# Kernel tuning notes

Hardware: AMD Instinct MI355X
Metric: run time of the kernel (lower is better)

The kernel has to match this reference:

```python
import jax, jax.numpy as jnp
import numpy as np

N_NODES = 200000
N_EDGES = 6400000
D_IN, D_HID, D_OUT = 128, 16, 172


def gcn_conv(x, edge_index, W, b, n):
    """PyG GCNConv: add self-loops, symmetric D^-1/2 A D^-1/2 normalization,
    linear projection, scatter-add aggregation, bias."""
    src, dst = edge_index[0], edge_index[1]
    loops = jnp.arange(n, dtype=edge_index.dtype)
    src = jnp.concatenate([src, loops])
    dst = jnp.concatenate([dst, loops])
    # in-degree with self-loops (>= 1, so rsqrt is safe)
    deg = jax.ops.segment_sum(jnp.ones_like(dst, dtype=x.dtype), dst, num_segments=n)
    dinv = jax.lax.rsqrt(deg)
    lin = x @ W  # [n, d_out]
    norm = dinv[src] * dinv[dst]  # per-edge normalization
    msg = lin[src] * norm[:, None]  # gather + scale
    out = jax.ops.segment_sum(msg, dst, num_segments=n)  # scatter-add
    return out + b


def setup_inputs() -> dict:
    key = jax.random.key(0)
    k1, k2, k3, k4, k5, k6 = jax.random.split(key, 6)
    x = jax.random.normal(k1, (N_NODES, D_IN), dtype=jnp.float32)
    edge_index = jax.random.randint(k2, (2, N_EDGES), 0, N_NODES, dtype=jnp.int64)
    W1 = jax.random.normal(k3, (D_IN, D_HID), dtype=jnp.float32) * (1.0 / np.sqrt(D_IN))
    b1 = jnp.zeros((D_HID,), dtype=jnp.float32)
    W2 = jax.random.normal(k4, (D_HID, D_OUT), dtype=jnp.float32) * (1.0 / np.sqrt(D_HID))
    b2 = jnp.zeros((D_OUT,), dtype=jnp.float32)
    return {"x": x, "edge_index": edge_index, "W1": W1, "b1": b1, "W2": W2, "b2": b2}


def reference(x, edge_index, W1, b1, W2, b2):
    n = x.shape[0]
    # CRD: GCNConv -> relu (dropout is identity in eval mode)
    h = jax.nn.relu(gcn_conv(x, edge_index, W1, b1, n))
    # CLS: GCNConv -> log_softmax over classes
    logits = gcn_conv(h, edge_index, W2, b2, n)
    return jax.nn.log_softmax(logits, axis=1)
```

## Files before the change

### kernel.cpp

```cpp
#include <hip/hip_runtime.h>
#include <hip/hip_fp16.h>

#define N_NODES 200000
#define N_EDGES 6400000
#define D_IN    128
#define D_HID   16
#define D_OUT   172

#define NS1     800
#define EPB     8000
#define SBN     782
#define SB_NODES 256

#define O_BTOT  0
#define O_BASE  1024
#define O_CNT1  2048
#define O_COL   2048
#define O_ROW   6402048
#define O_DINV  6602112
#define O_PACK  6802112
#define O_F16A  6802112
#define O_F16B  8402112
#define O_AGG2  10002112

__global__ __launch_bounds__(256) void k_hist1(const int* __restrict__ dst,
                                               unsigned* __restrict__ counts) {
    __shared__ unsigned cnt[SBN];
    for (int i = threadIdx.x; i < SBN; i += 256) cnt[i] = 0;
    __syncthreads();
    const int* dp = dst + blockIdx.x * EPB;
    for (int i = threadIdx.x; i < EPB; i += 256)
        atomicAdd(&cnt[dp[i] >> 8], 1u);
    __syncthreads();
    unsigned* out = counts + (size_t)blockIdx.x * SBN;
    for (int i = threadIdx.x; i < SBN; i += 256) out[i] = cnt[i];
}

__global__ __launch_bounds__(256) void k_scan_col(unsigned* __restrict__ counts,
                                                  unsigned* __restrict__ btot) {
    __shared__ unsigned arr[NS1];
    int b = blockIdx.x;
    for (int i = threadIdx.x; i < NS1; i += 256)
        arr[i] = counts[(size_t)i * SBN + b];
    __syncthreads();
    if (threadIdx.x < 64) {
        int l = threadIdx.x;
        int lo = l * 13, hi = min(lo + 13, NS1);
        unsigned sum = 0;
        for (int i = lo; i < hi; ++i) sum += arr[i];
        unsigned incl = sum;
#pragma unroll
        for (int o = 1; o < 64; o <<= 1) {
            unsigned tmp = __shfl_up(incl, o);
            if (l >= o) incl += tmp;
        }
        if (l == 63) btot[b] = incl;
        unsigned run = incl - sum;
        for (int i = lo; i < hi; ++i) { unsigned v = arr[i]; arr[i] = run; run += v; }
    }
    __syncthreads();
    for (int i = threadIdx.x; i < NS1; i += 256)
        counts[(size_t)i * SBN + b] = arr[i];
}

__global__ __launch_bounds__(64) void k_scan_base(const unsigned* __restrict__ btot,
                                                  unsigned* __restrict__ base) {
    int l = threadIdx.x;
    int lo = l * 13, hi = min(lo + 13, SBN);
    unsigned sum = 0;
    for (int i = lo; i < hi; ++i) sum += btot[i];
    unsigned incl = sum;
#pragma unroll
    for (int o = 1; o < 64; o <<= 1) {
        unsigned tmp = __shfl_up(incl, o);
        if (l >= o) incl += tmp;
    }
    unsigned run = incl - sum;
    for (int i = lo; i < hi; ++i) { unsigned v = btot[i]; base[i] = run; run += v; }
    if (l == 63) base[SBN] = incl;
}

__global__ __launch_bounds__(256) void k_scatter1(const int* __restrict__ src,
                                                  const int* __restrict__ dst,
                                                  const unsigned* __restrict__ counts,
                                                  const unsigned* __restrict__ base,
                                                  unsigned* __restrict__ packed) {
    __shared__ unsigned       sdat[EPB];
    __shared__ unsigned short sbkt[EPB];
    __shared__ unsigned cnt[SBN];
    __shared__ unsigned off[SBN];
    __shared__ unsigned gbs[SBN];
    __shared__ unsigned wsum[4];
    int t = threadIdx.x;
    const unsigned* crow = counts + (size_t)blockIdx.x * SBN;
    for (int i = t; i < SBN; i += 256) { cnt[i] = 0; gbs[i] = base[i] + crow[i]; }
    __syncthreads();
    const int* sp = src + blockIdx.x * EPB;
    const int* dp = dst + blockIdx.x * EPB;
    for (int i = t; i < EPB; i += 256) atomicAdd(&cnt[dp[i] >> 8], 1u);
    __syncthreads();
    int lane = t & 63, wid = t >> 6;
    int b0 = t * 4;
    unsigned c0v = (b0 + 0 < SBN) ? cnt[b0 + 0] : 0;
    unsigned c1v = (b0 + 1 < SBN) ? cnt[b0 + 1] : 0;
    unsigned c2v = (b0 + 2 < SBN) ? cnt[b0 + 2] : 0;
    unsigned c3v = (b0 + 3 < SBN) ? cnt[b0 + 3] : 0;
    unsigned mysum = c0v + c1v + c2v + c3v;
    unsigned incl = mysum;
#pragma unroll
    for (int o = 1; o < 64; o <<= 1) {
        unsigned tmp = __shfl_up(incl, o);
        if (lane >= o) incl += tmp;
    }
    if (lane == 63) wsum[wid] = incl;
    __syncthreads();
    unsigned wbase = 0;
    for (int w = 0; w < wid; ++w) wbase += wsum[w];
    unsigned run = wbase + incl - mysum;
    if (b0 + 0 < SBN) { off[b0 + 0] = run; run += c0v; }
    if (b0 + 1 < SBN) { off[b0 + 1] = run; run += c1v; }
    if (b0 + 2 < SBN) { off[b0 + 2] = run; run += c2v; }
    if (b0 + 3 < SBN) { off[b0 + 3] = run; run += c3v; }
    __syncthreads();
    for (int i = t; i < EPB; i += 256) {
        int s = sp[i], d = dp[i];
        unsigned b = (unsigned)d >> 8;
        unsigned slot = atomicAdd(&off[b], 1u);
        sdat[slot] = ((unsigned)(d & (SB_NODES - 1)) << 18) | (unsigned)s;
        sbkt[slot] = (unsigned short)b;
    }
    __syncthreads();
    for (int i = t; i < EPB; i += 256) {
        unsigned b = sbkt[i];
        unsigned start = off[b] - cnt[b];
        packed[gbs[b] + (i - start)] = sdat[i];
    }
}

__global__ __launch_bounds__(256) void k_csr(const unsigned* __restrict__ packed,
                                             const unsigned* __restrict__ base,
                                             int* __restrict__ rowptr,
                                             float* __restrict__ dinv,
                                             int* __restrict__ col) {
    __shared__ unsigned cnt[SB_NODES];
    __shared__ unsigned off[SB_NODES];
    __shared__ unsigned wsum[4];
    int t = threadIdx.x, sb = blockIdx.x;
    unsigned beg = base[sb], end = base[sb + 1];
    cnt[t] = 0;
    __syncthreads();
    for (unsigned i = beg + t; i < end; i += 256)
        atomicAdd(&cnt[packed[i] >> 18], 1u);
    __syncthreads();
    unsigned e = cnt[t];
    int lane = t & 63, wid = t >> 6;
    unsigned incl = e;
#pragma unroll
    for (int o = 1; o < 64; o <<= 1) {
        unsigned tmp = __shfl_up(incl, o);
        if (lane >= o) incl += tmp;
    }
    if (lane == 63) wsum[wid] = incl;
    __syncthreads();
    unsigned wbase = 0;
    for (int w = 0; w < wid; ++w) wbase += wsum[w];
    unsigned ex = wbase + incl - e;
    off[t] = ex;
    int n0 = sb * SB_NODES + t;
    if (n0 <= N_NODES) rowptr[n0] = (int)(beg + ex);
    if (n0 <  N_NODES) dinv[n0]   = rsqrtf((float)(e + 1));
    __syncthreads();
    for (unsigned i = beg + t; i < end; i += 256) {
        unsigned p = packed[i];
        unsigned slot = atomicAdd(&off[p >> 18], 1u);
        col[beg + slot] = (int)(p & 0x3FFFFu);
    }
}

__global__ __launch_bounds__(256) void k_lin1(const float* __restrict__ x,
                                              const float* __restrict__ W1,
                                              const float* __restrict__ dinv,
                                              __half* __restrict__ lin) {
    __shared__ float sW[D_IN * D_HID];
    for (int t = threadIdx.x; t < D_IN * D_HID; t += 256) sW[t] = W1[t];
    __syncthreads();

    int g  = threadIdx.x & 3;
    int nl = threadIdx.x >> 2;
    int n  = blockIdx.x * 64 + nl;

    float acc[16];
#pragma unroll
    for (int j = 0; j < 16; ++j) acc[j] = 0.f;

    const float4* xr = (const float4*)(x + (size_t)n * D_IN + g * 32);
#pragma unroll
    for (int i = 0; i < 8; ++i) {
        float4 xv = xr[i];
        int k = g * 32 + i * 4;
#pragma unroll
        for (int j = 0; j < 16; ++j) {
            acc[j] += xv.x * sW[(k + 0) * 16 + j] + xv.y * sW[(k + 1) * 16 + j]
                    + xv.z * sW[(k + 2) * 16 + j] + xv.w * sW[(k + 3) * 16 + j];
        }
    }
#pragma unroll
    for (int j = 0; j < 16; ++j) {
        acc[j] += __shfl_xor(acc[j], 1);
        acc[j] += __shfl_xor(acc[j], 2);
    }
    float di = dinv[n];
    ushort4 pk;
    pk.x = __half_as_ushort(__float2half(acc[g * 4 + 0] * di));
    pk.y = __half_as_ushort(__float2half(acc[g * 4 + 1] * di));
    pk.z = __half_as_ushort(__float2half(acc[g * 4 + 2] * di));
    pk.w = __half_as_ushort(__float2half(acc[g * 4 + 3] * di));
    *(ushort4*)(lin + (size_t)n * 16 + g * 4) = pk;
}

template <int MODE>
__global__ __launch_bounds__(256) void k_gather(const int* __restrict__ rowptr,
                                                const int* __restrict__ col,
                                                const float* __restrict__ dinv,
                                                const __half2* __restrict__ fin,
                                                const float* __restrict__ bias,
                                                void* __restrict__ outv) {
    int t = threadIdx.x;
    int n = blockIdx.x * 32 + (t >> 3);
    int lane = t & 7;
    int beg = rowptr[n], end = rowptr[n + 1];
    float2 a0 = __half22float2(fin[n * 8 + lane]);
    float2 a1 = {0,0}, a2 = {0,0}, a3 = {0,0};
    float2 a4 = {0,0}, a5 = {0,0}, a6 = {0,0}, a7 = {0,0};
    int i = beg;
    for (; i + 8 <= end; i += 8) {
        int s0 = col[i + 0], s1 = col[i + 1], s2 = col[i + 2], s3 = col[i + 3];
        int s4 = col[i + 4], s5 = col[i + 5], s6 = col[i + 6], s7 = col[i + 7];
        __half2 h0 = fin[s0 * 8 + lane], h1 = fin[s1 * 8 + lane];
        __half2 h2 = fin[s2 * 8 + lane], h3 = fin[s3 * 8 + lane];
        __half2 h4 = fin[s4 * 8 + lane], h5 = fin[s5 * 8 + lane];
        __half2 h6 = fin[s6 * 8 + lane], h7 = fin[s7 * 8 + lane];
        float2 f0 = __half22float2(h0), f1 = __half22float2(h1);
        float2 f2 = __half22float2(h2), f3 = __half22float2(h3);
        float2 f4 = __half22float2(h4), f5 = __half22float2(h5);
        float2 f6 = __half22float2(h6), f7 = __half22float2(h7);
        a0.x += f0.x; a0.y += f0.y;  a1.x += f1.x; a1.y += f1.y;
        a2.x += f2.x; a2.y += f2.y;  a3.x += f3.x; a3.y += f3.y;
        a4.x += f4.x; a4.y += f4.y;  a5.x += f5.x; a5.y += f5.y;
        a6.x += f6.x; a6.y += f6.y;  a7.x += f7.x; a7.y += f7.y;
    }
    for (; i < end; ++i) {
        float2 f = __half22float2(fin[col[i] * 8 + lane]);
        a0.x += f.x; a0.y += f.y;
    }
    float vx = ((a0.x + a1.x) + (a2.x + a3.x)) + ((a4.x + a5.x) + (a6.x + a7.x));
    float vy = ((a0.y + a1.y) + (a2.y + a3.y)) + ((a4.y + a5.y) + (a6.y + a7.y));
    float dd = dinv[n];
    vx *= dd; vy *= dd;
    if (MODE) {
        float2 b2v = ((const float2*)bias)[lane];
        vx = fmaxf(vx + b2v.x, 0.f) * dd;
        vy = fmaxf(vy + b2v.y, 0.f) * dd;
        ((__half2*)outv)[n * 8 + lane] = __floats2half2_rn(vx, vy);
    } else {
        ((float2*)outv)[n * 8 + lane] = make_float2(vx, vy);
    }
}

__global__ __launch_bounds__(256) void k_out(const float* __restrict__ agg2,
                                             const float* __restrict__ W2,
                                             const float* __restrict__ b2,
                                             float* __restrict__ out) {
    __shared__ float sWt[D_OUT * D_HID];
    __shared__ float sb[D_OUT];
    __shared__ float sl[64 * D_OUT];
    __shared__ float sls[64];
    int t = threadIdx.x;
    for (int m = t; m < D_OUT * D_HID; m += 256)
        sWt[m] = W2[(m & 15) * D_OUT + (m >> 4)];
    for (int m = t; m < D_OUT; m += 256) sb[m] = b2[m];
    __syncthreads();

    int nl = t >> 2, q = t & 3;
    int n  = blockIdx.x * 64 + nl;
    const float4* ar = (const float4*)(agg2 + (size_t)n * 16);
    float4 a0 = ar[0], a1 = ar[1], a2 = ar[2], a3 = ar[3];
    float a[16] = {a0.x, a0.y, a0.z, a0.w, a1.x, a1.y, a1.z, a1.w,
                   a2.x, a2.y, a2.z, a2.w, a3.x, a3.y, a3.z, a3.w};

    float mloc = -INFINITY;
    float* srow = sl + nl * D_OUT;
#pragma unroll 4
    for (int i = 0; i < 43; ++i) {
        int c = q + 4 * i;
        const float4* wr = (const float4*)(sWt + c * 16);
        float4 w0 = wr[0], w1 = wr[1], w2 = wr[2], w3 = wr[3];
        float l = sb[c];
        l += a[0]  * w0.x + a[1]  * w0.y + a[2]  * w0.z + a[3]  * w0.w;
        l += a[4]  * w1.x + a[5]  * w1.y + a[6]  * w1.z + a[7]  * w1.w;
        l += a[8]  * w2.x + a[9]  * w2.y + a[10] * w2.z + a[11] * w2.w;
        l += a[12] * w3.x + a[13] * w3.y + a[14] * w3.z + a[15] * w3.w;
        srow[c] = l;
        mloc = fmaxf(mloc, l);
    }
    mloc = fmaxf(mloc, __shfl_xor(mloc, 1));
    mloc = fmaxf(mloc, __shfl_xor(mloc, 2));
    float sloc = 0.f;
#pragma unroll 4
    for (int i = 0; i < 43; ++i) sloc += __expf(srow[q + 4 * i] - mloc);
    sloc += __shfl_xor(sloc, 1);
    sloc += __shfl_xor(sloc, 2);
    if (q == 0) sls[nl] = mloc + __logf(sloc);
    __syncthreads();

    const float4* sl4 = (const float4*)sl;
    float4* ob = (float4*)(out + (size_t)blockIdx.x * 64 * D_OUT);
    for (int jj = t; jj < 64 * D_OUT / 4; jj += 256) {
        float4 v = sl4[jj];
        float ls = sls[jj / 43];
        v.x -= ls; v.y -= ls; v.z -= ls; v.w -= ls;
        ob[jj] = v;
    }
}

extern "C" void kernel_launch(void* const* d_in, const int* in_sizes, int n_in,
                              void* d_out, int out_size, void* d_ws, size_t ws_size,
                              hipStream_t stream) {
    const float* x     = (const float*)d_in[0];
    const int*   edges = (const int*)d_in[1];
    const float* W1    = (const float*)d_in[2];
    const float* b1    = (const float*)d_in[3];
    const float* W2    = (const float*)d_in[4];
    const float* b2    = (const float*)d_in[5];
    float*       out   = (float*)d_out;

    const int* src = edges;
    const int* dst = edges + N_EDGES;

    unsigned* ws     = (unsigned*)d_ws;
    unsigned* btot   = ws + O_BTOT;
    unsigned* base   = ws + O_BASE;
    unsigned* counts = ws + O_CNT1;
    int*      col    = (int*)(ws + O_COL);
    int*      rowptr = (int*)(ws + O_ROW);
    float*    dinv   = (float*)(ws + O_DINV);
    unsigned* packed = ws + O_PACK;
    __half*   f16a   = (__half*)(ws + O_F16A);
    __half*   f16b   = (__half*)(ws + O_F16B);
    float*    agg2   = (float*)(ws + O_AGG2);

    k_hist1    <<<NS1, 256, 0, stream>>>(dst, counts);
    k_scan_col <<<SBN, 256, 0, stream>>>(counts, btot);
    k_scan_base<<<1,    64, 0, stream>>>(btot, base);
    k_scatter1 <<<NS1, 256, 0, stream>>>(src, dst, counts, base, packed);
    k_csr      <<<SBN, 256, 0, stream>>>(packed, base, rowptr, dinv, col);

    k_lin1     <<<N_NODES / 64, 256, 0, stream>>>(x, W1, dinv, f16a);
    k_gather<1><<<N_NODES / 32, 256, 0, stream>>>(rowptr, col, dinv,
                                                  (const __half2*)f16a, b1, f16b);

    k_gather<0><<<N_NODES / 32, 256, 0, stream>>>(rowptr, col, dinv,
                                                  (const __half2*)f16b, b1, agg2);
    k_out      <<<N_NODES / 64, 256, 0, stream>>>(agg2, W2, b2, out);
}
```

Before: 425.9 us.

## Remap k_out so each wave owns a class slice and uses online softmax

Rewrites the output kernel so each thread handles one node and each wavefront handles every fourth class. W2 and b2 are read as wave-uniform global loads instead of being staged transposed in shared memory. The row max and sum are computed in a single online log-sum-exp pass, and the four partial results are merged through shared memory. The logit tile row stride is padded to 173 to avoid LDS bank conflicts. This removes the W2 staging phase and the second exp pass over shared memory, at the cost of scalar per-element output stores in place of float4 stores, plus a conditional rescale exp per class.

```diff
diff --git a/kernel.cpp b/kernel.cpp
--- a/kernel.cpp
+++ b/kernel.cpp
@@ -267,59 +267,50 @@
     }
 }
 
+#define SLP 173
 __global__ __launch_bounds__(256) void k_out(const float* __restrict__ agg2,
                                              const float* __restrict__ W2,
                                              const float* __restrict__ b2,
                                              float* __restrict__ out) {
-    __shared__ float sWt[D_OUT * D_HID];
-    __shared__ float sb[D_OUT];
-    __shared__ float sl[64 * D_OUT];
+    __shared__ float sl[64 * SLP];
+    __shared__ float pm[4][64];
+    __shared__ float ps[4][64];
     __shared__ float sls[64];
-    int t = threadIdx.x;
-    for (int m = t; m < D_OUT * D_HID; m += 256)
-        sWt[m] = W2[(m & 15) * D_OUT + (m >> 4)];
-    for (int m = t; m < D_OUT; m += 256) sb[m] = b2[m];
-    __syncthreads();
-
-    int nl = t >> 2, q = t & 3;
-    int n  = blockIdx.x * 64 + nl;
+    int t   = threadIdx.x;
+    int wid = __builtin_amdgcn_readfirstlane(t >> 6);
+    int nl  = t & 63;
+    int n   = blockIdx.x * 64 + nl;
+
     const float4* ar = (const float4*)(agg2 + (size_t)n * 16);
     float4 a0 = ar[0], a1 = ar[1], a2 = ar[2], a3 = ar[3];
     float a[16] = {a0.x, a0.y, a0.z, a0.w, a1.x, a1.y, a1.z, a1.w,
                    a2.x, a2.y, a2.z, a2.w, a3.x, a3.y, a3.z, a3.w};
 
-    float mloc = -INFINITY;
-    float* srow = sl + nl * D_OUT;
-#pragma unroll 4
+    float m = -INFINITY, s = 0.f;
+    float* srow = sl + nl * SLP;
     for (int i = 0; i < 43; ++i) {
-        int c = q + 4 * i;
-        const float4* wr = (const float4*)(sWt + c * 16);
-        float4 w0 = wr[0], w1 = wr[1], w2 = wr[2], w3 = wr[3];
-        float l = sb[c];
-        l += a[0]  * w0.x + a[1]  * w0.y + a[2]  * w0.z + a[3]  * w0.w;
-        l += a[4]  * w1.x + a[5]  * w1.y + a[6]  * w1.z + a[7]  * w1.w;
-        l += a[8]  * w2.x + a[9]  * w2.y + a[10] * w2.z + a[11] * w2.w;
-        l += a[12] * w3.x + a[13] * w3.y + a[14] * w3.z + a[15] * w3.w;
+        int c = wid + 4 * i;
+        float l = b2[c];
+#pragma unroll
+        for (int k = 0; k < 16; ++k) l += a[k] * W2[k * D_OUT + c];
         srow[c] = l;
-        mloc = fmaxf(mloc, l);
-    }
-    mloc = fmaxf(mloc, __shfl_xor(mloc, 1));
-    mloc = fmaxf(mloc, __shfl_xor(mloc, 2));
-    float sloc = 0.f;
-#pragma unroll 4
-    for (int i = 0; i < 43; ++i) sloc += __expf(srow[q + 4 * i] - mloc);
-    sloc += __shfl_xor(sloc, 1);
-    sloc += __shfl_xor(sloc, 2);
-    if (q == 0) sls[nl] = mloc + __logf(sloc);
-    __syncthreads();
-
-    const float4* sl4 = (const float4*)sl;
-    float4* ob = (float4*)(out + (size_t)blockIdx.x * 64 * D_OUT);
-    for (int jj = t; jj < 64 * D_OUT / 4; jj += 256) {
-        float4 v = sl4[jj];
-        float ls = sls[jj / 43];
-        v.x -= ls; v.y -= ls; v.z -= ls; v.w -= ls;
-        ob[jj] = v;
+        if (l > m) { s *= __expf(m - l); m = l; }
+        s += __expf(l - m);
+    }
+    pm[wid][nl] = m; ps[wid][nl] = s;
+    __syncthreads();
+    if (wid == 0) {
+        float m0 = pm[0][nl], m1 = pm[1][nl], m2 = pm[2][nl], m3 = pm[3][nl];
+        float M  = fmaxf(fmaxf(m0, m1), fmaxf(m2, m3));
+        float S  = ps[0][nl] * __expf(m0 - M) + ps[1][nl] * __expf(m1 - M)
+                 + ps[2][nl] * __expf(m2 - M) + ps[3][nl] * __expf(m3 - M);
+        sls[nl] = M + __logf(S);
+    }
+    __syncthreads();
+    float* ob = out + (size_t)blockIdx.x * 64 * D_OUT;
+    for (int idx = t; idx < 64 * D_OUT; idx += 256) {
+        int node = idx / D_OUT, c = idx - node * D_OUT;
+        ob[idx] = sl[node * SLP + c] - sls[node];
     }
 }
 
```

After: 429.2 us. About the same (+0.8%).
